# Kernel tuning notes

Measured on AMD Instinct MI355X. Metric: run time of the kernel, lower is better.

The kernel has to match this reference:

```python
import jax, jax.numpy as jnp
import numpy as np
from jax import lax

# Cl(3,0) Cayley table: W_eff[i, j] = sum_k T[i, j, k] * w[k], signs transcribed
# verbatim from the 64 scatter ops in _cl300_expand_batched.
_TABLE = [
    [(0, 0, 1), (1, 1, 1), (2, 2, 1), (3, 3, 1), (4, 4, -1), (5, 5, -1), (6, 6, -1), (7, 7, -1)],
    [(1, 0, 1), (0, 1, 1), (4, 2, -1), (5, 3, -1), (2, 4, 1), (3, 5, 1), (7, 6, -1), (6, 7, -1)],
    [(2, 0, 1), (4, 1, 1), (0, 2, 1), (6, 3, -1), (1, 4, -1), (7, 5, 1), (3, 6, 1), (5, 7, 1)],
    [(3, 0, 1), (5, 1, 1), (6, 2, 1), (0, 3, 1), (7, 4, -1), (1, 5, -1), (2, 6, -1), (4, 7, -1)],
    [(4, 0, 1), (2, 1, 1), (1, 2, -1), (7, 3, 1), (0, 4, 1), (6, 5, -1), (5, 6, 1), (3, 7, 1)],
    [(5, 0, 1), (3, 1, 1), (7, 2, -1), (1, 3, -1), (6, 4, 1), (0, 5, 1), (4, 6, -1), (2, 7, -1)],
    [(6, 0, 1), (7, 1, 1), (3, 2, 1), (2, 3, -1), (5, 4, -1), (4, 5, 1), (0, 6, 1), (1, 7, 1)],
    [(7, 0, 1), (6, 1, 1), (5, 2, -1), (4, 3, 1), (3, 4, 1), (2, 5, -1), (1, 6, 1), (0, 7, 1)],
]

def _cayley():
    T = np.zeros((8, 8, 8), np.float32)
    for i, row in enumerate(_TABLE):
        for j, k, s in row:
            T[i, j, k] = s
    return jnp.asarray(T)


def setup_inputs() -> dict:
    key = jax.random.key(0)
    k0, k1 = jax.random.split(key, 2)
    B, F, P, G = 16, 8, 4, 32
    state = jax.random.normal(k0, (B, F, 8, G, G, G), jnp.float32)
    all_weights = jax.random.normal(k1, (F, P, 27, 8), jnp.float32) * 0.05
    # mimic _init_weights: zero the center tap, identity-ish on pass 0
    all_weights = all_weights.at[:, :, 26, :].set(0.0).at[:, 0, 26, 0].set(0.8)
    all_biases = jnp.zeros((F, P, 8), jnp.float32)
    field_mix_logits = jnp.tile(jnp.eye(F, dtype=jnp.float32) * 3.0, (P, 1, 1))
    pass_alpha_logit = jnp.full((P,), -1.0, jnp.float32)
    gate_weight = jnp.full((F, 8), 0.1, jnp.float32)
    gate_bias = jnp.full((F, 8), 2.0, jnp.float32)
    return dict(state=state, all_weights=all_weights, all_biases=all_biases,
                field_mix_logits=field_mix_logits, pass_alpha_logit=pass_alpha_logit,
                gate_weight=gate_weight, gate_bias=gate_bias)


def reference(state, all_weights, all_biases, field_mix_logits,
              pass_alpha_logit, gate_weight, gate_bias):
    B, F, _, G, _, _ = state.shape
    P = all_weights.shape[1]
    G3 = G * G * G
    T = _cayley()
    # sparse signed Cayley expansion: [F,P,27,8] -> [F,P,8,8,3,3,3]
    W_eff = jnp.einsum('ijk,fpck->fpijc', T, all_weights).reshape(F, P, 8, 8, 3, 3, 3)
    mix_all = jax.nn.softmax(field_mix_logits, axis=2)  # [P,F,F]
    x = state
    old_state = state
    for p in range(P):
        x_before = x
        Wg = W_eff[:, p].reshape(F * 8, 8, 3, 3, 3)
        bg = all_biases[:, p].reshape(F * 8)
        xf = x.reshape(B, F * 8, G, G, G)
        # causal shifted conv: asymmetric pad (2,0) per spatial dim, grouped by field
        y = lax.conv_general_dilated(
            xf, Wg, window_strides=(1, 1, 1), padding=[(2, 0), (2, 0), (2, 0)],
            dimension_numbers=('NCDHW', 'OIDHW', 'NCDHW'), feature_group_count=F)
        y = jnp.tanh(y + bg[None, :, None, None, None])  # [B,F*8,G,G,G]
        # cross-field mixing (bmm with shared mix matrix)
        xm = jnp.einsum('gf,bfm->bgm', mix_all[p], y.reshape(B, F, 8 * G3))
        x = xm.reshape(B, F, 8, G, G, G)
        alpha = jax.nn.sigmoid(pass_alpha_logit[p])
        x = alpha * x_before + (1.0 - alpha) * x
    gw = gate_weight.reshape(1, F, 8, 1, 1, 1)
    gb = gate_bias.reshape(1, F, 8, 1, 1, 1)
    gate = jax.nn.sigmoid(gw * old_state + gb)
    return gate * old_state + (1.0 - gate) * x
```

## Files before the change

kernel.cpp:

```cpp
#include <hip/hip_runtime.h>
#include <math.h>

#define B_  16
#define F_  8
#define C_  8
#define G_  32
#define G3_ 32768
#define P_  4
#define N_  (B_*F_*C_*G3_)
#define SF_ (C_*G3_)
#define SB_ (F_*SF_)
#define APACK_SZ (P_*F_*9*64*8)

typedef __attribute__((ext_vector_type(8))) short short8v;
typedef __attribute__((ext_vector_type(4))) float f32x4;
typedef unsigned short u16;
typedef unsigned int u32;

__device__ __constant__ int c_k[8][8] = {
  {0,1,2,3,4,5,6,7},
  {1,0,4,5,2,3,7,6},
  {2,4,0,6,1,7,3,5},
  {3,5,6,0,7,1,2,4},
  {4,2,1,7,0,6,5,3},
  {5,3,7,1,6,0,4,2},
  {6,7,3,2,5,4,0,1},
  {7,6,5,4,3,2,1,0}};
__device__ __constant__ float c_s[8][8] = {
  { 1, 1, 1, 1,-1,-1,-1,-1},
  { 1, 1, 1, 1,-1,-1,-1,-1},
  { 1,-1, 1, 1, 1, 1,-1, 1},
  { 1,-1,-1, 1,-1, 1, 1,-1},
  { 1,-1, 1, 1, 1, 1,-1, 1},
  { 1,-1,-1, 1,-1, 1, 1,-1},
  { 1, 1,-1, 1, 1,-1, 1, 1},
  { 1, 1,-1, 1, 1,-1, 1, 1}};

__device__ __forceinline__ float fast_tanh(float v) {
  float e = __expf(2.f * v);
  return 1.f - 2.f / (e + 1.f);
}
__device__ __forceinline__ float fast_sig(float v) {
  return 1.f / (1.f + __expf(-v));
}
__device__ __forceinline__ u32 bf16_rne(float v) {
  u32 u = __float_as_uint(v);
  return (u + 0x7FFFu + ((u >> 16) & 1u)) >> 16;
}
__device__ __forceinline__ u32 pk_bf16(float a, float b) {
  u32 d;
  asm("v_cvt_pk_bf16_f32 %0, %1, %2" : "=v"(d) : "v"(a), "v"(b));
  return d;
}
__device__ __forceinline__ float bl(u32 u) { return __uint_as_float(u << 16); }
__device__ __forceinline__ float bh(u32 u) { return __uint_as_float(u & 0xffff0000u); }

#define HS(pt) (((pt) + ((pt) >> 2)) & 3)
#define OSTR 34

__global__ void prep_kernel(const float* __restrict__ all_weights,
                            const float* __restrict__ mix_logits,
                            u16* __restrict__ Apack,
                            float* __restrict__ mix) {
  int idx = blockIdx.x * 256 + threadIdx.x;
  if (idx < APACK_SZ) {
    int e = idx & 7;
    int l = (idx >> 3) & 63;
    int rest = idx >> 9;
    int t = rest % 9;
    int fp = rest / 9;
    int f = fp & 7, p = fp >> 3;
    int g = l >> 4, m = l & 15;
    int zoff = m >> 3, i = m & 7;
    int kk = g*4 + (e & 3) + ((e >= 4) ? 16 : 0);
    int zl = kk >> 3, j = kk & 7;
    int dz = zl - zoff;
    float val = 0.f;
    if (dz >= 0 && dz <= 2)
      val = c_s[i][j] * all_weights[((f*P_ + p)*27 + (dz*9 + t))*8 + c_k[i][j]];
    Apack[idx] = (u16)bf16_rne(val);
  }
  if (blockIdx.x == 0 && threadIdx.x < P_*F_) {
    int p = threadIdx.x / F_, g = threadIdx.x % F_;
    const float* row = &mix_logits[(p*F_ + g)*F_];
    float mx = row[0];
    for (int f = 1; f < F_; ++f) mx = fmaxf(mx, row[f]);
    float e[F_]; float sum = 0.f;
    for (int f = 0; f < F_; ++f) { e[f] = __expf(row[f] - mx); sum += e[f]; }
    float inv = 1.f / sum;
    for (int f = 0; f < F_; ++f) mix[(p*F_ + g)*F_ + f] = e[f] * inv;
  }
}

#define TPTS 204

template<int MODE>
__device__ __forceinline__ uint4 field_step(
    int f, const void* __restrict__ xsrc_, const u16* __restrict__ Apack,
    const float* __restrict__ biases, int p, int b, int z0, int y0,
    u32* xk, int tid, int lane, int wid, int g, int ln) {
  if (f) __syncthreads();

  if (tid < 192) {
    int qq  = tid / 48;
    int r2  = tid - qq*48;
    int row = r2 >> 3;
    int c   = r2 & 7;
    int zl = qq >> 1, jq = qq & 1;
    int gz0 = z0 - 2 + zl;
    int gy  = y0 - 2 + row;
    int gx  = c * 4;
    int off = (jq*4)*G3_ + gz0*1024 + gy*32 + gx;
    int ptb = row*34 + 2 + gx;
    u32 d0[4], d1[4], d2[4], d3[4];
    if (MODE != 0) {
      const u16* s0 = (const u16*)xsrc_ + (size_t)b*SB_ + f*SF_ + off;
      const u16* s1 = s0 + 2048;
      uint2 a0={0,0},a1={0,0},a2={0,0},a3={0,0};
      uint2 e0={0,0},e1={0,0},e2={0,0},e3={0,0};
      if (gy >= 0) {
        if (gz0 >= 0) {
          a0 = *(const uint2*)(s0);
          a1 = *(const uint2*)(s0 + G3_);
          a2 = *(const uint2*)(s0 + 2*G3_);
          a3 = *(const uint2*)(s0 + 3*G3_);
        }
        e0 = *(const uint2*)(s1);
        e1 = *(const uint2*)(s1 + G3_);
        e2 = *(const uint2*)(s1 + 2*G3_);
        e3 = *(const uint2*)(s1 + 3*G3_);
      }
      d0[0] = __builtin_amdgcn_perm(a1.x, a0.x, 0x05040100u);
      d0[1] = __builtin_amdgcn_perm(a1.x, a0.x, 0x07060302u);
      d0[2] = __builtin_amdgcn_perm(a1.y, a0.y, 0x05040100u);
      d0[3] = __builtin_amdgcn_perm(a1.y, a0.y, 0x07060302u);
      d1[0] = __builtin_amdgcn_perm(a3.x, a2.x, 0x05040100u);
      d1[1] = __builtin_amdgcn_perm(a3.x, a2.x, 0x07060302u);
      d1[2] = __builtin_amdgcn_perm(a3.y, a2.y, 0x05040100u);
      d1[3] = __builtin_amdgcn_perm(a3.y, a2.y, 0x07060302u);
      d2[0] = __builtin_amdgcn_perm(e1.x, e0.x, 0x05040100u);
      d2[1] = __builtin_amdgcn_perm(e1.x, e0.x, 0x07060302u);
      d2[2] = __builtin_amdgcn_perm(e1.y, e0.y, 0x05040100u);
      d2[3] = __builtin_amdgcn_perm(e1.y, e0.y, 0x07060302u);
      d3[0] = __builtin_amdgcn_perm(e3.x, e2.x, 0x05040100u);
      d3[1] = __builtin_amdgcn_perm(e3.x, e2.x, 0x07060302u);
      d3[2] = __builtin_amdgcn_perm(e3.y, e2.y, 0x05040100u);
      d3[3] = __builtin_amdgcn_perm(e3.y, e2.y, 0x07060302u);
    } else {
      const float* s0 = (const float*)xsrc_ + (size_t)b*SB_ + f*SF_ + off;
      const float* s1 = s0 + 2048;
      float4 A0={0,0,0,0},A1={0,0,0,0},A2={0,0,0,0},A3={0,0,0,0};
      float4 B0={0,0,0,0},B1={0,0,0,0},B2={0,0,0,0},B3={0,0,0,0};
      if (gy >= 0) {
        if (gz0 >= 0) {
          A0 = *(const float4*)(s0);
          A1 = *(const float4*)(s0 + G3_);
          A2 = *(const float4*)(s0 + 2*G3_);
          A3 = *(const float4*)(s0 + 3*G3_);
        }
        B0 = *(const float4*)(s1);
        B1 = *(const float4*)(s1 + G3_);
        B2 = *(const float4*)(s1 + 2*G3_);
        B3 = *(const float4*)(s1 + 3*G3_);
      }
      d0[0]=pk_bf16(A0.x,A1.x); d1[0]=pk_bf16(A2.x,A3.x);
      d2[0]=pk_bf16(B0.x,B1.x); d3[0]=pk_bf16(B2.x,B3.x);
      d0[1]=pk_bf16(A0.y,A1.y); d1[1]=pk_bf16(A2.y,A3.y);
      d2[1]=pk_bf16(B0.y,B1.y); d3[1]=pk_bf16(B2.y,B3.y);
      d0[2]=pk_bf16(A0.z,A1.z); d1[2]=pk_bf16(A2.z,A3.z);
      d2[2]=pk_bf16(B0.z,B1.z); d3[2]=pk_bf16(B2.z,B3.z);
      d0[3]=pk_bf16(A0.w,A1.w); d1[3]=pk_bf16(A2.w,A3.w);
      d2[3]=pk_bf16(B0.w,B1.w); d3[3]=pk_bf16(B2.w,B3.w);
    }
    #define STW(px) { \
      uint4 d; d.x = d0[px]; d.y = d1[px]; d.z = d2[px]; d.w = d3[px]; \
      int pt = ptb + px; \
      *(uint4*)&xk[pt*16 + ((qq ^ HS(pt)) << 2)] = d; }
    STW(0) STW(1) STW(2) STW(3)
    #undef STW
  }

  short8v a[9];
  const u16* ap = Apack + (size_t)((p*8 + f) * 9) * 512;
  #pragma unroll
  for (int t = 0; t < 9; ++t)
    a[t] = *(const short8v*)(ap + (t*64 + lane)*8);

  __syncthreads();

  f32x4 acc0 = {0.f,0.f,0.f,0.f}, acc1 = {0.f,0.f,0.f,0.f};
  #pragma unroll
  for (int dy = 0; dy < 3; ++dy) {
    int prow = (wid + dy)*34;
    #pragma unroll
    for (int dx = 0; dx < 3; ++dx) {
      int t = dy*3 + dx;
      int pt0 = prow + ln + dx;
      int dwb = pt0*16 + ((g ^ HS(pt0)) << 2);
      short8v b0 = *(const short8v*)&xk[dwb];
      short8v b1 = *(const short8v*)&xk[dwb + 256];
      acc0 = __builtin_amdgcn_mfma_f32_16x16x32_bf16(a[t], b0, acc0, 0, 0, 0);
      acc1 = __builtin_amdgcn_mfma_f32_16x16x32_bf16(a[t], b1, acc1, 0, 0, 0);
    }
  }

  const float* bb = biases + (f*P_ + p)*8 + (g & 1)*4;
  float b0v = bb[0], b1v = bb[1], b2v = bb[2], b3v = bb[3];
  uint4 yp;
  yp.x = pk_bf16(fast_tanh(acc0[0] + b0v), fast_tanh(acc0[1] + b1v));
  yp.y = pk_bf16(fast_tanh(acc0[2] + b2v), fast_tanh(acc0[3] + b3v));
  yp.z = pk_bf16(fast_tanh(acc1[0] + b0v), fast_tanh(acc1[1] + b1v));
  yp.w = pk_bf16(fast_tanh(acc1[2] + b2v), fast_tanh(acc1[3] + b3v));
  return yp;
}

template<int MODE>
__global__ __launch_bounds__(256, 4)
void fused_kernel(const void* __restrict__ xsrc_,
                  void* __restrict__ xdst_,
                  const float* __restrict__ state,
                  const u16* __restrict__ Apack,
                  const float* __restrict__ biases,
                  const float* __restrict__ mixb,
                  const float* __restrict__ pal,
                  const float* __restrict__ gw,
                  const float* __restrict__ gb,
                  int p) {
  __shared__ __align__(16) u32 xk[TPTS * 16];
  __shared__ __align__(16) float obuf[4][16*OSTR];

  int bid = blockIdx.x;
  int yt = bid & 7;
  int zt = (bid >> 3) & 15;
  int b  =  bid >> 7;
  int z0 = zt * 2, y0 = yt * 4;
  int tid  = threadIdx.x;
  int lane = tid & 63;
  int wid  = tid >> 6;
  int g    = lane >> 4;
  int ln   = lane & 15;

  if (tid < 192) {
    int pt = (tid >> 5) * 34 + ((tid >> 4) & 1);
    xk[pt*16 + (tid & 15)] = 0u;
  }

  uint4 yp0 = field_step<MODE>(0, xsrc_, Apack, biases, p, b, z0, y0, xk, tid, lane, wid, g, ln);
  uint4 yp1 = field_step<MODE>(1, xsrc_, Apack, biases, p, b, z0, y0, xk, tid, lane, wid, g, ln);
  uint4 yp2 = field_step<MODE>(2, xsrc_, Apack, biases, p, b, z0, y0, xk, tid, lane, wid, g, ln);
  uint4 yp3 = field_step<MODE>(3, xsrc_, Apack, biases, p, b, z0, y0, xk, tid, lane, wid, g, ln);
  uint4 yp4 = field_step<MODE>(4, xsrc_, Apack, biases, p, b, z0, y0, xk, tid, lane, wid, g, ln);
  uint4 yp5 = field_step<MODE>(5, xsrc_, Apack, biases, p, b, z0, y0, xk, tid, lane, wid, g, ln);
  uint4 yp6 = field_step<MODE>(6, xsrc_, Apack, biases, p, b, z0, y0, xk, tid, lane, wid, g, ln);
  uint4 yp7 = field_step<MODE>(7, xsrc_, Apack, biases, p, b, z0, y0, xk, tid, lane, wid, g, ln);

  float alpha = fast_sig(pal[p]);
  float na = 1.f - alpha;
  int zoff = g >> 1;
  int i0 = (g & 1)*4;

  float* ob = &obuf[wid][0];
  int srow = lane >> 2;
  int sc   = srow >> 1, sz = srow & 1;
  int sx   = (lane & 3) * 8;
  size_t sbase = (size_t)b*SB_ + (size_t)sc*G3_ + (size_t)(z0 + sz)*1024
               + (size_t)(y0 + wid)*32 + sx;

  #pragma unroll
  for (int gg = 0; gg < 8; ++gg) {
    const float* mr = mixb + (p*8 + gg)*8;
    float o[8] = {0.f,0.f,0.f,0.f,0.f,0.f,0.f,0.f};
    #define MIXF(F, YPV) { \
      float m = mr[F]; \
      o[0] = fmaf(m, bl(YPV.x), o[0]); o[1] = fmaf(m, bh(YPV.x), o[1]); \
      o[2] = fmaf(m, bl(YPV.y), o[2]); o[3] = fmaf(m, bh(YPV.y), o[3]); \
      o[4] = fmaf(m, bl(YPV.z), o[4]); o[5] = fmaf(m, bh(YPV.z), o[5]); \
      o[6] = fmaf(m, bl(YPV.w), o[6]); o[7] = fmaf(m, bh(YPV.w), o[7]); }
    MIXF(0, yp0) MIXF(1, yp1) MIXF(2, yp2) MIXF(3, yp3)
    MIXF(4, yp4) MIXF(5, yp5) MIXF(6, yp6) MIXF(7, yp7)
    #undef MIXF

    #pragma unroll
    for (int e = 0; e < 8; ++e)
      ob[((i0 + (e & 3))*2 + zoff)*OSTR + ln + ((e >> 2) << 4)] = o[e];

    float4 m0 = *(const float4*)&ob[srow*OSTR + sx];
    float4 m1 = *(const float4*)&ob[srow*OSTR + sx + 4];

    size_t sidx = sbase + (size_t)gg*SF_;
    float xb[8], xf[8];
    if (MODE == 0) {
      const float* xsp = (const float*)xsrc_ + sidx;
      float4 x0 = *(const float4*)(xsp);
      float4 x1 = *(const float4*)(xsp + 4);
      xb[0]=x0.x; xb[1]=x0.y; xb[2]=x0.z; xb[3]=x0.w;
      xb[4]=x1.x; xb[5]=x1.y; xb[6]=x1.z; xb[7]=x1.w;
    } else {
      uint4 u = *(const uint4*)((const u16*)xsrc_ + sidx);
      xb[0]=bl(u.x); xb[1]=bh(u.x); xb[2]=bl(u.y); xb[3]=bh(u.y);
      xb[4]=bl(u.z); xb[5]=bh(u.z); xb[6]=bl(u.w); xb[7]=bh(u.w);
    }
    float mv[8] = {m0.x,m0.y,m0.z,m0.w, m1.x,m1.y,m1.z,m1.w};
    #pragma unroll
    for (int e = 0; e < 8; ++e) xf[e] = alpha*xb[e] + na*mv[e];

    if (MODE == 2) {
      const float* stp = state + sidx;
      float4 s0 = *(const float4*)(stp);
      float4 s1 = *(const float4*)(stp + 4);
      float st[8] = {s0.x,s0.y,s0.z,s0.w, s1.x,s1.y,s1.z,s1.w};
      float w  = gw[gg*8 + sc];
      float bv = gb[gg*8 + sc];
      float r[8];
      #pragma unroll
      for (int e = 0; e < 8; ++e) {
        float gt = fast_sig(w*st[e] + bv);
        r[e] = gt*st[e] + (1.f - gt)*xf[e];
      }
      float* op = (float*)xdst_ + sidx;
      *(float4*)(op)     = make_float4(r[0],r[1],r[2],r[3]);
      *(float4*)(op + 4) = make_float4(r[4],r[5],r[6],r[7]);
    } else {
      uint4 w;
      w.x = pk_bf16(xf[0], xf[1]);
      w.y = pk_bf16(xf[2], xf[3]);
      w.z = pk_bf16(xf[4], xf[5]);
      w.w = pk_bf16(xf[6], xf[7]);
      *(uint4*)((u16*)xdst_ + sidx) = w;
    }
  }
}

extern "C" void kernel_launch(void* const* d_in, const int* in_sizes, int n_in,
                              void* d_out, int out_size, void* d_ws, size_t ws_size,
                              hipStream_t stream) {
  (void)in_sizes; (void)n_in; (void)out_size; (void)ws_size;
  const float* state       = (const float*)d_in[0];
  const float* all_weights = (const float*)d_in[1];
  const float* all_biases  = (const float*)d_in[2];
  const float* mix_logits  = (const float*)d_in[3];
  const float* pal         = (const float*)d_in[4];
  const float* gw          = (const float*)d_in[5];
  const float* gb          = (const float*)d_in[6];
  float* out = (float*)d_out;

  u16* X0 = (u16*)d_ws;
  u16* X1 = X0 + N_;
  u16* Apack = X1 + N_;
  float* mixb = (float*)(Apack + APACK_SZ);

  prep_kernel<<<dim3(APACK_SZ/256), dim3(256), 0, stream>>>(
      all_weights, mix_logits, Apack, mixb);

  dim3 grid(2048), blk(256);
  fused_kernel<0><<<grid, blk, 0, stream>>>((const void*)state, (void*)X0, state,
      Apack, all_biases, mixb, pal, gw, gb, 0);
  fused_kernel<1><<<grid, blk, 0, stream>>>((const void*)X0, (void*)X1, state,
      Apack, all_biases, mixb, pal, gw, gb, 1);
  fused_kernel<1><<<grid, blk, 0, stream>>>((const void*)X1, (void*)X0, state,
      Apack, all_biases, mixb, pal, gw, gb, 2);
  fused_kernel<2><<<grid, blk, 0, stream>>>((const void*)X0, (void*)out, state,
      Apack, all_biases, mixb, pal, gw, gb, 3);
}
```

Before: 292.9 us.

## Double-buffer LDS tiles and prefetch next field's loads during MFMA compute

```diff
diff --git a/kernel.cpp b/kernel.cpp
--- a/kernel.cpp
+++ b/kernel.cpp
@@ -57,6 +57,7 @@
 
 #define HS(pt) (((pt) + ((pt) >> 2)) & 3)
 #define OSTR 34
+#define TPTS 204
 
 __global__ void prep_kernel(const float* __restrict__ all_weights,
                             const float* __restrict__ mix_logits,
@@ -92,101 +93,115 @@
   }
 }
 
-#define TPTS 204
+struct LdRegs {
+  uint2 a0,a1,a2,a3,e0,e1,e2,e3;
+  float4 f0,f1,f2,f3,f4,f5,f6,f7;
+};
 
 template<int MODE>
-__device__ __forceinline__ uint4 field_step(
-    int f, const void* __restrict__ xsrc_, const u16* __restrict__ Apack,
-    const float* __restrict__ biases, int p, int b, int z0, int y0,
-    u32* xk, int tid, int lane, int wid, int g, int ln) {
-  if (f) __syncthreads();
-
-  if (tid < 192) {
-    int qq  = tid / 48;
-    int r2  = tid - qq*48;
-    int row = r2 >> 3;
-    int c   = r2 & 7;
-    int zl = qq >> 1, jq = qq & 1;
-    int gz0 = z0 - 2 + zl;
-    int gy  = y0 - 2 + row;
-    int gx  = c * 4;
-    int off = (jq*4)*G3_ + gz0*1024 + gy*32 + gx;
-    int ptb = row*34 + 2 + gx;
-    u32 d0[4], d1[4], d2[4], d3[4];
-    if (MODE != 0) {
-      const u16* s0 = (const u16*)xsrc_ + (size_t)b*SB_ + f*SF_ + off;
-      const u16* s1 = s0 + 2048;
-      uint2 a0={0,0},a1={0,0},a2={0,0},a3={0,0};
-      uint2 e0={0,0},e1={0,0},e2={0,0},e3={0,0};
-      if (gy >= 0) {
-        if (gz0 >= 0) {
-          a0 = *(const uint2*)(s0);
-          a1 = *(const uint2*)(s0 + G3_);
-          a2 = *(const uint2*)(s0 + 2*G3_);
-          a3 = *(const uint2*)(s0 + 3*G3_);
-        }
-        e0 = *(const uint2*)(s1);
-        e1 = *(const uint2*)(s1 + G3_);
-        e2 = *(const uint2*)(s1 + 2*G3_);
-        e3 = *(const uint2*)(s1 + 3*G3_);
+__device__ __forceinline__ void stage_load(
+    int f, const void* __restrict__ xsrc_, int b, int z0, int y0, int tid,
+    LdRegs& r) {
+  if (tid >= 192) return;
+  int qq  = tid / 48;
+  int r2  = tid - qq*48;
+  int row = r2 >> 3;
+  int c   = r2 & 7;
+  int zl = qq >> 1, jq = qq & 1;
+  int gz0 = z0 - 2 + zl;
+  int gy  = y0 - 2 + row;
+  int gx  = c * 4;
+  int off = (jq*4)*G3_ + gz0*1024 + gy*32 + gx;
+  if (MODE != 0) {
+    const u16* s0 = (const u16*)xsrc_ + (size_t)b*SB_ + f*SF_ + off;
+    const u16* s1 = s0 + 2048;
+    r.a0 = r.a1 = r.a2 = r.a3 = make_uint2(0,0);
+    r.e0 = r.e1 = r.e2 = r.e3 = make_uint2(0,0);
+    if (gy >= 0) {
+      if (gz0 >= 0) {
+        r.a0 = *(const uint2*)(s0);
+        r.a1 = *(const uint2*)(s0 + G3_);
+        r.a2 = *(const uint2*)(s0 + 2*G3_);
+        r.a3 = *(const uint2*)(s0 + 3*G3_);
       }
-      d0[0] = __builtin_amdgcn_perm(a1.x, a0.x, 0x05040100u);
-      d0[1] = __builtin_amdgcn_perm(a1.x, a0.x, 0x07060302u);
-      d0[2] = __builtin_amdgcn_perm(a1.y, a0.y, 0x05040100u);
-      d0[3] = __builtin_amdgcn_perm(a1.y, a0.y, 0x07060302u);
-      d1[0] = __builtin_amdgcn_perm(a3.x, a2.x, 0x05040100u);
-      d1[1] = __builtin_amdgcn_perm(a3.x, a2.x, 0x07060302u);
-      d1[2] = __builtin_amdgcn_perm(a3.y, a2.y, 0x05040100u);
-      d1[3] = __builtin_amdgcn_perm(a3.y, a2.y, 0x07060302u);
-      d2[0] = __builtin_amdgcn_perm(e1.x, e0.x, 0x05040100u);
-      d2[1] = __builtin_amdgcn_perm(e1.x, e0.x, 0x07060302u);
-      d2[2] = __builtin_amdgcn_perm(e1.y, e0.y, 0x05040100u);
-      d2[3] = __builtin_amdgcn_perm(e1.y, e0.y, 0x07060302u);
-      d3[0] = __builtin_amdgcn_perm(e3.x, e2.x, 0x05040100u);
-      d3[1] = __builtin_amdgcn_perm(e3.x, e2.x, 0x07060302u);
-      d3[2] = __builtin_amdgcn_perm(e3.y, e2.y, 0x05040100u);
-      d3[3] = __builtin_amdgcn_perm(e3.y, e2.y, 0x07060302u);
-    } else {
-      const float* s0 = (const float*)xsrc_ + (size_t)b*SB_ + f*SF_ + off;
-      const float* s1 = s0 + 2048;
-      float4 A0={0,0,0,0},A1={0,0,0,0},A2={0,0,0,0},A3={0,0,0,0};
-      float4 B0={0,0,0,0},B1={0,0,0,0},B2={0,0,0,0},B3={0,0,0,0};
-      if (gy >= 0) {
-        if (gz0 >= 0) {
-          A0 = *(const float4*)(s0);
-          A1 = *(const float4*)(s0 + G3_);
-          A2 = *(const float4*)(s0 + 2*G3_);
-          A3 = *(const float4*)(s0 + 3*G3_);
-        }
-        B0 = *(const float4*)(s1);
-        B1 = *(const float4*)(s1 + G3_);
-        B2 = *(const float4*)(s1 + 2*G3_);
-        B3 = *(const float4*)(s1 + 3*G3_);
+      r.e0 = *(const uint2*)(s1);
+      r.e1 = *(const uint2*)(s1 + G3_);
+      r.e2 = *(const uint2*)(s1 + 2*G3_);
+      r.e3 = *(const uint2*)(s1 + 3*G3_);
+    }
+  } else {
+    const float* s0 = (const float*)xsrc_ + (size_t)b*SB_ + f*SF_ + off;
+    const float* s1 = s0 + 2048;
+    float4 z4 = {0,0,0,0};
+    r.f0=r.f1=r.f2=r.f3=z4; r.f4=r.f5=r.f6=r.f7=z4;
+    if (gy >= 0) {
+      if (gz0 >= 0) {
+        r.f0 = *(const float4*)(s0);
+        r.f1 = *(const float4*)(s0 + G3_);
+        r.f2 = *(const float4*)(s0 + 2*G3_);
+        r.f3 = *(const float4*)(s0 + 3*G3_);
       }
-      d0[0]=pk_bf16(A0.x,A1.x); d1[0]=pk_bf16(A2.x,A3.x);
-      d2[0]=pk_bf16(B0.x,B1.x); d3[0]=pk_bf16(B2.x,B3.x);
-      d0[1]=pk_bf16(A0.y,A1.y); d1[1]=pk_bf16(A2.y,A3.y);
-      d2[1]=pk_bf16(B0.y,B1.y); d3[1]=pk_bf16(B2.y,B3.y);
-      d0[2]=pk_bf16(A0.z,A1.z); d1[2]=pk_bf16(A2.z,A3.z);
-      d2[2]=pk_bf16(B0.z,B1.z); d3[2]=pk_bf16(B2.z,B3.z);
-      d0[3]=pk_bf16(A0.w,A1.w); d1[3]=pk_bf16(A2.w,A3.w);
-      d2[3]=pk_bf16(B0.w,B1.w); d3[3]=pk_bf16(B2.w,B3.w);
+      r.f4 = *(const float4*)(s1);
+      r.f5 = *(const float4*)(s1 + G3_);
+      r.f6 = *(const float4*)(s1 + 2*G3_);
+      r.f7 = *(const float4*)(s1 + 3*G3_);
     }
-    #define STW(px) { \
-      uint4 d; d.x = d0[px]; d.y = d1[px]; d.z = d2[px]; d.w = d3[px]; \
-      int pt = ptb + px; \
-      *(uint4*)&xk[pt*16 + ((qq ^ HS(pt)) << 2)] = d; }
-    STW(0) STW(1) STW(2) STW(3)
-    #undef STW
-  }
-
+  }
+}
+
+template<int MODE>
+__device__ __forceinline__ void stage_write(u32* xk, int tid, const LdRegs& r) {
+  if (tid >= 192) return;
+  int qq  = tid / 48;
+  int r2  = tid - qq*48;
+  int row = r2 >> 3;
+  int c   = r2 & 7;
+  int gx  = c * 4;
+  int ptb = row*34 + 2 + gx;
+  u32 d0[4], d1[4], d2[4], d3[4];
+  if (MODE != 0) {
+    d0[0] = __builtin_amdgcn_perm(r.a1.x, r.a0.x, 0x05040100u);
+    d0[1] = __builtin_amdgcn_perm(r.a1.x, r.a0.x, 0x07060302u);
+    d0[2] = __builtin_amdgcn_perm(r.a1.y, r.a0.y, 0x05040100u);
+    d0[3] = __builtin_amdgcn_perm(r.a1.y, r.a0.y, 0x07060302u);
+    d1[0] = __builtin_amdgcn_perm(r.a3.x, r.a2.x, 0x05040100u);
+    d1[1] = __builtin_amdgcn_perm(r.a3.x, r.a2.x, 0x07060302u);
+    d1[2] = __builtin_amdgcn_perm(r.a3.y, r.a2.y, 0x05040100u);
+    d1[3] = __builtin_amdgcn_perm(r.a3.y, r.a2.y, 0x07060302u);
+    d2[0] = __builtin_amdgcn_perm(r.e1.x, r.e0.x, 0x05040100u);
+    d2[1] = __builtin_amdgcn_perm(r.e1.x, r.e0.x, 0x07060302u);
+    d2[2] = __builtin_amdgcn_perm(r.e1.y, r.e0.y, 0x05040100u);
+    d2[3] = __builtin_amdgcn_perm(r.e1.y, r.e0.y, 0x07060302u);
+    d3[0] = __builtin_amdgcn_perm(r.e3.x, r.e2.x, 0x05040100u);
+    d3[1] = __builtin_amdgcn_perm(r.e3.x, r.e2.x, 0x07060302u);
+    d3[2] = __builtin_amdgcn_perm(r.e3.y, r.e2.y, 0x05040100u);
+    d3[3] = __builtin_amdgcn_perm(r.e3.y, r.e2.y, 0x07060302u);
+  } else {
+    d0[0]=pk_bf16(r.f0.x,r.f1.x); d1[0]=pk_bf16(r.f2.x,r.f3.x);
+    d2[0]=pk_bf16(r.f4.x,r.f5.x); d3[0]=pk_bf16(r.f6.x,r.f7.x);
+    d0[1]=pk_bf16(r.f0.y,r.f1.y); d1[1]=pk_bf16(r.f2.y,r.f3.y);
+    d2[1]=pk_bf16(r.f4.y,r.f5.y); d3[1]=pk_bf16(r.f6.y,r.f7.y);
+    d0[2]=pk_bf16(r.f0.z,r.f1.z); d1[2]=pk_bf16(r.f2.z,r.f3.z);
+    d2[2]=pk_bf16(r.f4.z,r.f5.z); d3[2]=pk_bf16(r.f6.z,r.f7.z);
+    d0[3]=pk_bf16(r.f0.w,r.f1.w); d1[3]=pk_bf16(r.f2.w,r.f3.w);
+    d2[3]=pk_bf16(r.f4.w,r.f5.w); d3[3]=pk_bf16(r.f6.w,r.f7.w);
+  }
+  #define STW(px) { \
+    uint4 d; d.x = d0[px]; d.y = d1[px]; d.z = d2[px]; d.w = d3[px]; \
+    int pt = ptb + px; \
+    *(uint4*)&xk[pt*16 + ((qq ^ HS(pt)) << 2)] = d; }
+  STW(0) STW(1) STW(2) STW(3)
+  #undef STW
+}
+
+__device__ __forceinline__ uint4 conv_compute(
+    int f, const u16* __restrict__ Apack, const float* __restrict__ biases,
+    int p, const u32* xk, int lane, int wid, int g, int ln) {
   short8v a[9];
   const u16* ap = Apack + (size_t)((p*8 + f) * 9) * 512;
   #pragma unroll
   for (int t = 0; t < 9; ++t)
     a[t] = *(const short8v*)(ap + (t*64 + lane)*8);
-
-  __syncthreads();
 
   f32x4 acc0 = {0.f,0.f,0.f,0.f}, acc1 = {0.f,0.f,0.f,0.f};
   #pragma unroll
@@ -226,7 +241,8 @@
                   const float* __restrict__ gw,
                   const float* __restrict__ gb,
                   int p) {
-  __shared__ __align__(16) u32 xk[TPTS * 16];
+  __shared__ __align__(16) u32 xk0[TPTS * 16];
+  __shared__ __align__(16) u32 xk1[TPTS * 16];
   __shared__ __align__(16) float obuf[4][16*OSTR];
 
   int bid = blockIdx.x;
@@ -242,23 +258,50 @@
 
   if (tid < 192) {
     int pt = (tid >> 5) * 34 + ((tid >> 4) & 1);
-    xk[pt*16 + (tid & 15)] = 0u;
-  }
-
-  uint4 yp0 = field_step<MODE>(0, xsrc_, Apack, biases, p, b, z0, y0, xk, tid, lane, wid, g, ln);
-  uint4 yp1 = field_step<MODE>(1, xsrc_, Apack, biases, p, b, z0, y0, xk, tid, lane, wid, g, ln);
-  uint4 yp2 = field_step<MODE>(2, xsrc_, Apack, biases, p, b, z0, y0, xk, tid, lane, wid, g, ln);
-  uint4 yp3 = field_step<MODE>(3, xsrc_, Apack, biases, p, b, z0, y0, xk, tid, lane, wid, g, ln);
-  uint4 yp4 = field_step<MODE>(4, xsrc_, Apack, biases, p, b, z0, y0, xk, tid, lane, wid, g, ln);
-  uint4 yp5 = field_step<MODE>(5, xsrc_, Apack, biases, p, b, z0, y0, xk, tid, lane, wid, g, ln);
-  uint4 yp6 = field_step<MODE>(6, xsrc_, Apack, biases, p, b, z0, y0, xk, tid, lane, wid, g, ln);
-  uint4 yp7 = field_step<MODE>(7, xsrc_, Apack, biases, p, b, z0, y0, xk, tid, lane, wid, g, ln);
+    xk0[pt*16 + (tid & 15)] = 0u;
+    xk1[pt*16 + (tid & 15)] = 0u;
+  }
+
+  LdRegs r;
+  stage_load<MODE>(0, xsrc_, b, z0, y0, tid, r);
+  stage_write<MODE>(xk0, tid, r);
+  stage_load<MODE>(1, xsrc_, b, z0, y0, tid, r);
+  __syncthreads();
+
+  uint4 yp0, yp1, yp2, yp3, yp4, yp5, yp6, yp7;
+  yp0 = conv_compute(0, Apack, biases, p, xk0, lane, wid, g, ln);
+  stage_write<MODE>(xk1, tid, r);
+  stage_load<MODE>(2, xsrc_, b, z0, y0, tid, r);
+  __syncthreads();
+  yp1 = conv_compute(1, Apack, biases, p, xk1, lane, wid, g, ln);
+  stage_write<MODE>(xk0, tid, r);
+  stage_load<MODE>(3, xsrc_, b, z0, y0, tid, r);
+  __syncthreads();
+  yp2 = conv_compute(2, Apack, biases, p, xk0, lane, wid, g, ln);
+  stage_write<MODE>(xk1, tid, r);
+  stage_load<MODE>(4, xsrc_, b, z0, y0, tid, r);
+  __syncthreads();
+  yp3 = conv_compute(3, Apack, biases, p, xk1, lane, wid, g, ln);
+  stage_write<MODE>(xk0, tid, r);
+  stage_load<MODE>(5, xsrc_, b, z0, y0, tid, r);
+  __syncthreads();
+  yp4 = conv_compute(4, Apack, biases, p, xk0, lane, wid, g, ln);
+  stage_write<MODE>(xk1, tid, r);
+  stage_load<MODE>(6, xsrc_, b, z0, y0, tid, r);
+  __syncthreads();
+  yp5 = conv_compute(5, Apack, biases, p, xk1, lane, wid, g, ln);
+  stage_write<MODE>(xk0, tid, r);
+  stage_load<MODE>(7, xsrc_, b, z0, y0, tid, r);
+  __syncthreads();
+  yp6 = conv_compute(6, Apack, biases, p, xk0, lane, wid, g, ln);
+  stage_write<MODE>(xk1, tid, r);
+  __syncthreads();
+  yp7 = conv_compute(7, Apack, biases, p, xk1, lane, wid, g, ln);
 
   float alpha = fast_sig(pal[p]);
   float na = 1.f - alpha;
   int zoff = g >> 1;
   int i0 = (g & 1)*4;
-
   float* ob = &obuf[wid][0];
   int srow = lane >> 2;
   int sc   = srow >> 1, sz = srow & 1;
@@ -311,15 +354,15 @@
       float st[8] = {s0.x,s0.y,s0.z,s0.w, s1.x,s1.y,s1.z,s1.w};
       float w  = gw[gg*8 + sc];
       float bv = gb[gg*8 + sc];
-      float r[8];
+      float rr[8];
       #pragma unroll
       for (int e = 0; e < 8; ++e) {
         float gt = fast_sig(w*st[e] + bv);
-        r[e] = gt*st[e] + (1.f - gt)*xf[e];
+        rr[e] = gt*st[e] + (1.f - gt)*xf[e];
       }
       float* op = (float*)xdst_ + sidx;
-      *(float4*)(op)     = make_float4(r[0],r[1],r[2],r[3]);
-      *(float4*)(op + 4) = make_float4(r[4],r[5],r[6],r[7]);
+      *(float4*)(op)     = make_float4(rr[0],rr[1],rr[2],rr[3]);
+      *(float4*)(op + 4) = make_float4(rr[4],rr[5],rr[6],rr[7]);
     } else {
       uint4 w;
       w.x = pk_bf16(xf[0], xf[1]);
```

Result: slower. 302.3 us (+3.2%).
